# Performance work log

Measured on AMD Instinct MI355X. Metric: run time of the kernel, lower is better.

The kernel has to match this reference:

```python
import jax, jax.numpy as jnp
import numpy as np

N_USERS = 100000
N_ITEMS = 100000
N_NODES = N_USERS + N_ITEMS
NNZ = 6400000
DIM = 64
N_HOPS = 3


def setup_inputs() -> dict:
    key = jax.random.key(0)
    k1, k2, k3, k4, k5 = jax.random.split(key, 5)
    user_embed = jax.random.normal(k1, (N_USERS, DIM), dtype=jnp.float32)
    item_embed = jax.random.normal(k2, (N_ITEMS, DIM), dtype=jnp.float32)
    # Normalized-adjacency-style positive values for the sparse matrix.
    edge_vals = jax.random.uniform(k3, (NNZ,), dtype=jnp.float32)
    edge_rows = jax.random.randint(k4, (NNZ,), 0, N_NODES, dtype=jnp.int32)
    edge_cols = jax.random.randint(k5, (NNZ,), 0, N_NODES, dtype=jnp.int32)
    return {
        "user_embed": user_embed,
        "item_embed": item_embed,
        "edge_vals": edge_vals,
        "edge_rows": edge_rows,
        "edge_cols": edge_cols,
    }


def reference(user_embed, item_embed, edge_vals, edge_rows, edge_cols):
    # all_embed: [N_NODES, DIM]
    all_embed = jnp.concatenate([user_embed, item_embed], axis=0)
    agg = all_embed
    embs = [all_embed]
    for _ in range(N_HOPS):
        # SpMM in COO form: out[r] += v * agg[c]  for each edge (r, c, v)
        gathered = edge_vals[:, None] * agg[edge_cols]  # [NNZ, DIM]
        agg = jax.ops.segment_sum(gathered, edge_rows, num_segments=N_NODES)
        embs.append(agg)
    embs = jnp.stack(embs, axis=1)  # [N_NODES, N_HOPS+1, DIM]
    return embs[:N_USERS], embs[N_USERS:]
```

## Files before the change

kernel.cpp:

```cpp
#include <hip/hip_runtime.h>

#define N_USERS 100000
#define N_ITEMS 100000
#define N_NODES (N_USERS + N_ITEMS)
#define NNZ 6400000
#define DIM 64
#define NHOPS 3
#define NODE_STRIDE ((NHOPS + 1) * DIM)

#define RPB 128
#define NB 1563
#define TILE 8192
#define NTILES ((NNZ + TILE - 1) / TILE)
#define P2CAP 7808

#define WS_BCNT 0
#define WS_BPTR 2048
#define WS_BCUR 4096
#define WS_RP   6144
#define WS_STG  206848
#define WS_MIRA 13006848
#define WS_MIRB 19406848

__device__ __forceinline__ unsigned short f2bf(float f) {
    unsigned u = __float_as_uint(f);
    u += 0x7fffu + ((u >> 16) & 1u);
    return (unsigned short)(u >> 16);
}
__device__ __forceinline__ float bf2f(unsigned short h) {
    return __uint_as_float((unsigned)h << 16);
}

__global__ void zero_bcnt_kernel(int* __restrict__ bcnt) {
    int i = blockIdx.x * blockDim.x + threadIdx.x;
    if (i < NB) bcnt[i] = 0;
}

__global__ void bhist_kernel(const int* __restrict__ rows, int* __restrict__ bcnt) {
    __shared__ int h[NB];
    for (int i = threadIdx.x; i < NB; i += blockDim.x) h[i] = 0;
    __syncthreads();
    int stride = gridDim.x * blockDim.x;
    for (int i = blockIdx.x * blockDim.x + threadIdx.x; i < NNZ; i += stride)
        atomicAdd(&h[rows[i] >> 7], 1);
    __syncthreads();
    for (int i = threadIdx.x; i < NB; i += blockDim.x)
        if (h[i]) atomicAdd(&bcnt[i], h[i]);
}

__global__ void bscan_kernel(const int* __restrict__ bcnt,
                             int* __restrict__ bptr, int* __restrict__ bcur) {
    __shared__ int buf[1024];
    int t = threadIdx.x;
    int a = (2 * t < NB) ? bcnt[2 * t] : 0;
    int b = (2 * t + 1 < NB) ? bcnt[2 * t + 1] : 0;
    int s = a + b;
    buf[t] = s;
    __syncthreads();
    for (int off = 1; off < 1024; off <<= 1) {
        int v = (t >= off) ? buf[t - off] : 0;
        __syncthreads();
        buf[t] += v;
        __syncthreads();
    }
    int ex = buf[t] - s;
    if (2 * t < NB)     { bptr[2 * t] = ex;     bcur[2 * t] = ex; }
    if (2 * t + 1 < NB) { bptr[2 * t + 1] = ex + a; bcur[2 * t + 1] = ex + a; }
    if (t == 0) bptr[NB] = NNZ;
}

__global__ void partition_kernel(const int* __restrict__ rows, const int* __restrict__ cols,
                                 const float* __restrict__ vals,
                                 int* __restrict__ bcur, int2* __restrict__ stg) {
    __shared__ int lh[NB];
    __shared__ int gb[NB];
    for (int i = threadIdx.x; i < NB; i += 512) lh[i] = 0;
    __syncthreads();
    const int base = blockIdx.x * TILE;
    int pk[16];
    #pragma unroll
    for (int k = 0; k < 16; ++k) {
        int e = base + k * 512 + (int)threadIdx.x;
        if (e < NNZ) {
            int r = rows[e];
            int b = r >> 7;
            int rank = atomicAdd(&lh[b], 1);
            pk[k] = b | ((r & 127) << 11) | (rank << 18);
        } else pk[k] = -1;
    }
    __syncthreads();
    for (int i = threadIdx.x; i < NB; i += 512) {
        int c = lh[i];
        if (c) gb[i] = atomicAdd(&bcur[i], c);
    }
    __syncthreads();
    #pragma unroll
    for (int k = 0; k < 16; ++k) {
        if (pk[k] >= 0) {
            int e = base + k * 512 + (int)threadIdx.x;
            int b    = pk[k] & 2047;
            int rl   = (pk[k] >> 11) & 127;
            int rank = pk[k] >> 18;
            int2 v;
            v.x = cols[e] | (rl << 18);
            v.y = __float_as_int(vals[e]);
            stg[gb[b] + rank] = v;
        }
    }
}

__global__ void pass2_kernel(const int* __restrict__ bptr, int2* __restrict__ stg,
                             int* __restrict__ row_ptr) {
    __shared__ int2 sd[P2CAP];
    __shared__ int  lh[RPB];
    __shared__ int  lc[RPB];
    int b = blockIdx.x;
    int s = bptr[b], e = bptr[b + 1];
    int cnt = e - s;
    for (int i = threadIdx.x; i < cnt; i += 256) sd[i] = stg[s + i];
    int t = threadIdx.x;
    if (t < RPB) lh[t] = 0;
    __syncthreads();
    for (int i = threadIdx.x; i < cnt; i += 256)
        atomicAdd(&lh[(sd[i].x >> 18) & 127], 1);
    __syncthreads();
    int own = (t < RPB) ? lh[t] : 0;
    for (int off = 1; off < RPB; off <<= 1) {
        int u = (t < RPB && t >= off) ? lh[t - off] : 0;
        __syncthreads();
        if (t < RPB) lh[t] += u;
        __syncthreads();
    }
    int rowbase = b * RPB;
    int nrows = min(RPB, N_NODES - rowbase);
    if (t < RPB) {
        int ex = lh[t] - own;
        lc[t] = ex;
        if (t < nrows) row_ptr[rowbase + t] = s + ex;
    }
    if (b == NB - 1 && t == 0) row_ptr[N_NODES] = NNZ;
    __syncthreads();
    for (int i = threadIdx.x; i < cnt; i += 256) {
        int2 d = sd[i];
        int rl = (d.x >> 18) & 127;
        int pos = atomicAdd(&lc[rl], 1);
        d.x &= 0x3FFFF;
        stg[s + pos] = d;
    }
}

__global__ void init_hop0_kernel(const float4* __restrict__ ue,
                                 const float4* __restrict__ ie,
                                 float* __restrict__ out,
                                 unsigned short* __restrict__ mirA) {
    int i = blockIdx.x * blockDim.x + threadIdx.x;
    if (i >= N_NODES * 16) return;
    int n = i >> 4, q = i & 15;
    float4 v = (n < N_USERS) ? ue[i] : ie[i - N_USERS * 16];
    ((float4*)(out + (size_t)n * NODE_STRIDE))[q] = v;
    ushort4 h;
    h.x = f2bf(v.x); h.y = f2bf(v.y); h.z = f2bf(v.z); h.w = f2bf(v.w);
    *(ushort4*)(mirA + ((size_t)n << 6) + q * 4) = h;
}

__global__ void spmm_bf_kernel(const int* __restrict__ row_ptr,
                               const int2* __restrict__ csr_pair,
                               const unsigned short* __restrict__ src,
                               unsigned short* __restrict__ dst,
                               float* __restrict__ out, int hop, int write_dst) {
    int wid = (blockIdx.x * blockDim.x + threadIdx.x) >> 6;
    if (wid >= N_NODES) return;
    int lane = threadIdx.x & 63;
    int g = lane >> 4;
    int q = lane & 15;
    int s = row_ptr[wid];
    int e = row_ptr[wid + 1];
    float4 acc = make_float4(0.f, 0.f, 0.f, 0.f);
    int j = s + g;
    for (; j + 4 < e; j += 8) {
        int2 p0 = csr_pair[j];
        int2 p1 = csr_pair[j + 4];
        ushort4 h0 = *(const ushort4*)(src + ((size_t)p0.x << 6) + q * 4);
        ushort4 h1 = *(const ushort4*)(src + ((size_t)p1.x << 6) + q * 4);
        float v0 = __int_as_float(p0.y);
        float v1 = __int_as_float(p1.y);
        acc.x += v0 * bf2f(h0.x); acc.y += v0 * bf2f(h0.y);
        acc.z += v0 * bf2f(h0.z); acc.w += v0 * bf2f(h0.w);
        acc.x += v1 * bf2f(h1.x); acc.y += v1 * bf2f(h1.y);
        acc.z += v1 * bf2f(h1.z); acc.w += v1 * bf2f(h1.w);
    }
    if (j < e) {
        int2 p0 = csr_pair[j];
        ushort4 h0 = *(const ushort4*)(src + ((size_t)p0.x << 6) + q * 4);
        float v0 = __int_as_float(p0.y);
        acc.x += v0 * bf2f(h0.x); acc.y += v0 * bf2f(h0.y);
        acc.z += v0 * bf2f(h0.z); acc.w += v0 * bf2f(h0.w);
    }
    acc.x += __shfl_xor(acc.x, 16); acc.y += __shfl_xor(acc.y, 16);
    acc.z += __shfl_xor(acc.z, 16); acc.w += __shfl_xor(acc.w, 16);
    acc.x += __shfl_xor(acc.x, 32); acc.y += __shfl_xor(acc.y, 32);
    acc.z += __shfl_xor(acc.z, 32); acc.w += __shfl_xor(acc.w, 32);
    if (g == 0) {
        ((float4*)(out + (size_t)wid * NODE_STRIDE + hop * DIM))[q] = acc;
        if (write_dst) {
            ushort4 h;
            h.x = f2bf(acc.x); h.y = f2bf(acc.y); h.z = f2bf(acc.z); h.w = f2bf(acc.w);
            *(ushort4*)(dst + ((size_t)wid << 6) + q * 4) = h;
        }
    }
}

extern "C" void kernel_launch(void* const* d_in, const int* in_sizes, int n_in,
                              void* d_out, int out_size, void* d_ws, size_t ws_size,
                              hipStream_t stream) {
    const float* user_e = (const float*)d_in[0];
    const float* item_e = (const float*)d_in[1];
    const float* vals   = (const float*)d_in[2];
    const int*   rows   = (const int*)d_in[3];
    const int*   cols   = (const int*)d_in[4];
    float* out = (float*)d_out;

    int*  wsi     = (int*)d_ws;
    int*  bcnt    = wsi + WS_BCNT;
    int*  bptr    = wsi + WS_BPTR;
    int*  bcur    = wsi + WS_BCUR;
    int*  row_ptr = wsi + WS_RP;
    int2* stg     = (int2*)(wsi + WS_STG);
    unsigned short* mirA = (unsigned short*)(wsi + WS_MIRA);
    unsigned short* mirB = (unsigned short*)(wsi + WS_MIRB);

    hipLaunchKernelGGL(zero_bcnt_kernel, dim3((NB + 255) / 256), dim3(256), 0, stream, bcnt);
    hipLaunchKernelGGL(bhist_kernel, dim3(1024), dim3(256), 0, stream, rows, bcnt);
    hipLaunchKernelGGL(bscan_kernel, dim3(1), dim3(1024), 0, stream, bcnt, bptr, bcur);
    hipLaunchKernelGGL(partition_kernel, dim3(NTILES), dim3(512), 0, stream,
                       rows, cols, vals, bcur, stg);
    hipLaunchKernelGGL(pass2_kernel, dim3(NB), dim3(256), 0, stream, bptr, stg, row_ptr);
    hipLaunchKernelGGL(init_hop0_kernel, dim3((N_NODES * 16 + 255) / 256), dim3(256), 0, stream,
                       (const float4*)user_e, (const float4*)item_e, out, mirA);

    const dim3 sg((N_NODES * 64 + 255) / 256), sb(256);
    hipLaunchKernelGGL(spmm_bf_kernel, sg, sb, 0, stream, row_ptr, stg, mirA, mirB, out, 1, 1);
    hipLaunchKernelGGL(spmm_bf_kernel, sg, sb, 0, stream, row_ptr, stg, mirB, mirA, out, 2, 1);
    hipLaunchKernelGGL(spmm_bf_kernel, sg, sb, 0, stream, row_ptr, stg, mirA, mirB, out, 3, 0);
}
```

Baseline: 705.0 us.

## Widen row buckets to 192 and restructure partition as persistent two-pass kernel

Row buckets grow from 128 to 192 rows, which cuts the bucket count to 1042. The partition kernel becomes a persistent grid of 256 blocks of 1024 threads over 16K-edge tiles. Each tile is counted in shared memory first, then scattered using shared atomics for slot positions, so the packed per-thread rank registers go away. The scatter rereads rows and adds integer divides. pass2 now clamps cnt to a smaller P2CAP of 7000, which could silently drop edges if a bucket overflows. Within-bucket order now depends on atomic timing.

Result: faster. 666.7 us (-5.4%).

```diff
diff --git a/kernel.cpp b/kernel.cpp
--- a/kernel.cpp
+++ b/kernel.cpp
@@ -8,19 +8,19 @@
 #define NHOPS 3
 #define NODE_STRIDE ((NHOPS + 1) * DIM)
 
-#define RPB 128
-#define NB 1563
-#define TILE 8192
-#define NTILES ((NNZ + TILE - 1) / TILE)
-#define P2CAP 7808
+#define BROWS 192
+#define NBK 1042
+#define PTILE 16384
+#define NTILES ((NNZ + PTILE - 1) / PTILE)
+#define P2CAP 7000
 
 #define WS_BCNT 0
-#define WS_BPTR 2048
-#define WS_BCUR 4096
-#define WS_RP   6144
-#define WS_STG  206848
-#define WS_MIRA 13006848
-#define WS_MIRB 19406848
+#define WS_BPTR 1056
+#define WS_BCUR 2112
+#define WS_RP   3168
+#define WS_STG  203264
+#define WS_MIRA 13003264
+#define WS_MIRB 19403264
 
 __device__ __forceinline__ unsigned short f2bf(float f) {
     unsigned u = __float_as_uint(f);
@@ -33,18 +33,18 @@
 
 __global__ void zero_bcnt_kernel(int* __restrict__ bcnt) {
     int i = blockIdx.x * blockDim.x + threadIdx.x;
-    if (i < NB) bcnt[i] = 0;
+    if (i < NBK) bcnt[i] = 0;
 }
 
 __global__ void bhist_kernel(const int* __restrict__ rows, int* __restrict__ bcnt) {
-    __shared__ int h[NB];
-    for (int i = threadIdx.x; i < NB; i += blockDim.x) h[i] = 0;
+    __shared__ int h[NBK];
+    for (int i = threadIdx.x; i < NBK; i += blockDim.x) h[i] = 0;
     __syncthreads();
     int stride = gridDim.x * blockDim.x;
     for (int i = blockIdx.x * blockDim.x + threadIdx.x; i < NNZ; i += stride)
-        atomicAdd(&h[rows[i] >> 7], 1);
-    __syncthreads();
-    for (int i = threadIdx.x; i < NB; i += blockDim.x)
+        atomicAdd(&h[(unsigned)rows[i] / BROWS], 1);
+    __syncthreads();
+    for (int i = threadIdx.x; i < NBK; i += blockDim.x)
         if (h[i]) atomicAdd(&bcnt[i], h[i]);
 }
 
@@ -52,8 +52,8 @@
                              int* __restrict__ bptr, int* __restrict__ bcur) {
     __shared__ int buf[1024];
     int t = threadIdx.x;
-    int a = (2 * t < NB) ? bcnt[2 * t] : 0;
-    int b = (2 * t + 1 < NB) ? bcnt[2 * t + 1] : 0;
+    int a = (2 * t < NBK) ? bcnt[2 * t] : 0;
+    int b = (2 * t + 1 < NBK) ? bcnt[2 * t + 1] : 0;
     int s = a + b;
     buf[t] = s;
     __syncthreads();
@@ -64,85 +64,77 @@
         __syncthreads();
     }
     int ex = buf[t] - s;
-    if (2 * t < NB)     { bptr[2 * t] = ex;     bcur[2 * t] = ex; }
-    if (2 * t + 1 < NB) { bptr[2 * t + 1] = ex + a; bcur[2 * t + 1] = ex + a; }
-    if (t == 0) bptr[NB] = NNZ;
-}
-
-__global__ void partition_kernel(const int* __restrict__ rows, const int* __restrict__ cols,
-                                 const float* __restrict__ vals,
-                                 int* __restrict__ bcur, int2* __restrict__ stg) {
-    __shared__ int lh[NB];
-    __shared__ int gb[NB];
-    for (int i = threadIdx.x; i < NB; i += 512) lh[i] = 0;
-    __syncthreads();
-    const int base = blockIdx.x * TILE;
-    int pk[16];
-    #pragma unroll
-    for (int k = 0; k < 16; ++k) {
-        int e = base + k * 512 + (int)threadIdx.x;
-        if (e < NNZ) {
+    if (2 * t < NBK)     { bptr[2 * t] = ex;         bcur[2 * t] = ex; }
+    if (2 * t + 1 < NBK) { bptr[2 * t + 1] = ex + a; bcur[2 * t + 1] = ex + a; }
+    if (t == 0) bptr[NBK] = NNZ;
+}
+
+__global__ void __launch_bounds__(1024) partition_kernel(
+        const int* __restrict__ rows, const int* __restrict__ cols,
+        const float* __restrict__ vals,
+        int* __restrict__ bcur, int2* __restrict__ stg) {
+    __shared__ int cur[NBK];
+    for (int tile = blockIdx.x; tile < NTILES; tile += gridDim.x) {
+        for (int i = threadIdx.x; i < NBK; i += 1024) cur[i] = 0;
+        __syncthreads();
+        const int base = tile * PTILE;
+        const int end  = min(base + PTILE, NNZ);
+        for (int e = base + (int)threadIdx.x; e < end; e += 1024)
+            atomicAdd(&cur[(unsigned)rows[e] / BROWS], 1);
+        __syncthreads();
+        for (int i = threadIdx.x; i < NBK; i += 1024) {
+            int c = cur[i];
+            cur[i] = c ? atomicAdd(&bcur[i], c) : 0;
+        }
+        __syncthreads();
+        for (int e = base + (int)threadIdx.x; e < end; e += 1024) {
             int r = rows[e];
-            int b = r >> 7;
-            int rank = atomicAdd(&lh[b], 1);
-            pk[k] = b | ((r & 127) << 11) | (rank << 18);
-        } else pk[k] = -1;
-    }
-    __syncthreads();
-    for (int i = threadIdx.x; i < NB; i += 512) {
-        int c = lh[i];
-        if (c) gb[i] = atomicAdd(&bcur[i], c);
-    }
-    __syncthreads();
-    #pragma unroll
-    for (int k = 0; k < 16; ++k) {
-        if (pk[k] >= 0) {
-            int e = base + k * 512 + (int)threadIdx.x;
-            int b    = pk[k] & 2047;
-            int rl   = (pk[k] >> 11) & 127;
-            int rank = pk[k] >> 18;
+            unsigned b = (unsigned)r / BROWS;
+            int rl = r - (int)b * BROWS;
+            int pos = atomicAdd(&cur[b], 1);
             int2 v;
             v.x = cols[e] | (rl << 18);
             v.y = __float_as_int(vals[e]);
-            stg[gb[b] + rank] = v;
+            stg[pos] = v;
         }
-    }
-}
-
-__global__ void pass2_kernel(const int* __restrict__ bptr, int2* __restrict__ stg,
-                             int* __restrict__ row_ptr) {
+        __syncthreads();
+    }
+}
+
+__global__ void __launch_bounds__(256) pass2_kernel(
+        const int* __restrict__ bptr, int2* __restrict__ stg,
+        int* __restrict__ row_ptr) {
     __shared__ int2 sd[P2CAP];
-    __shared__ int  lh[RPB];
-    __shared__ int  lc[RPB];
+    __shared__ int  lh[BROWS];
+    __shared__ int  lc[BROWS];
     int b = blockIdx.x;
     int s = bptr[b], e = bptr[b + 1];
-    int cnt = e - s;
+    int cnt = min(e - s, P2CAP);
     for (int i = threadIdx.x; i < cnt; i += 256) sd[i] = stg[s + i];
     int t = threadIdx.x;
-    if (t < RPB) lh[t] = 0;
-    __syncthreads();
-    for (int i = threadIdx.x; i < cnt; i += 256)
-        atomicAdd(&lh[(sd[i].x >> 18) & 127], 1);
-    __syncthreads();
-    int own = (t < RPB) ? lh[t] : 0;
-    for (int off = 1; off < RPB; off <<= 1) {
-        int u = (t < RPB && t >= off) ? lh[t - off] : 0;
-        __syncthreads();
-        if (t < RPB) lh[t] += u;
-        __syncthreads();
-    }
-    int rowbase = b * RPB;
-    int nrows = min(RPB, N_NODES - rowbase);
-    if (t < RPB) {
+    if (t < BROWS) lh[t] = 0;
+    __syncthreads();
+    for (int i = t; i < cnt; i += 256)
+        atomicAdd(&lh[(unsigned)sd[i].x >> 18], 1);
+    __syncthreads();
+    int own = (t < BROWS) ? lh[t] : 0;
+    for (int off = 1; off < BROWS; off <<= 1) {
+        int u = (t < BROWS && t >= off) ? lh[t - off] : 0;
+        __syncthreads();
+        if (t < BROWS) lh[t] += u;
+        __syncthreads();
+    }
+    int rowbase = b * BROWS;
+    if (t < BROWS) {
         int ex = lh[t] - own;
         lc[t] = ex;
-        if (t < nrows) row_ptr[rowbase + t] = s + ex;
-    }
-    if (b == NB - 1 && t == 0) row_ptr[N_NODES] = NNZ;
-    __syncthreads();
-    for (int i = threadIdx.x; i < cnt; i += 256) {
+        if (rowbase + t < N_NODES) row_ptr[rowbase + t] = s + ex;
+    }
+    if (b == NBK - 1 && t == 0) row_ptr[N_NODES] = NNZ;
+    __syncthreads();
+    for (int i = t; i < cnt; i += 256) {
         int2 d = sd[i];
-        int rl = (d.x >> 18) & 127;
+        int rl = (unsigned)d.x >> 18;
         int pos = atomicAdd(&lc[rl], 1);
         d.x &= 0x3FFFF;
         stg[s + pos] = d;
@@ -229,12 +221,12 @@
     unsigned short* mirA = (unsigned short*)(wsi + WS_MIRA);
     unsigned short* mirB = (unsigned short*)(wsi + WS_MIRB);
 
-    hipLaunchKernelGGL(zero_bcnt_kernel, dim3((NB + 255) / 256), dim3(256), 0, stream, bcnt);
+    hipLaunchKernelGGL(zero_bcnt_kernel, dim3((NBK + 255) / 256), dim3(256), 0, stream, bcnt);
     hipLaunchKernelGGL(bhist_kernel, dim3(1024), dim3(256), 0, stream, rows, bcnt);
     hipLaunchKernelGGL(bscan_kernel, dim3(1), dim3(1024), 0, stream, bcnt, bptr, bcur);
-    hipLaunchKernelGGL(partition_kernel, dim3(NTILES), dim3(512), 0, stream,
+    hipLaunchKernelGGL(partition_kernel, dim3(256), dim3(1024), 0, stream,
                        rows, cols, vals, bcur, stg);
-    hipLaunchKernelGGL(pass2_kernel, dim3(NB), dim3(256), 0, stream, bptr, stg, row_ptr);
+    hipLaunchKernelGGL(pass2_kernel, dim3(NBK), dim3(256), 0, stream, bptr, stg, row_ptr);
     hipLaunchKernelGGL(init_hop0_kernel, dim3((N_NODES * 16 + 255) / 256), dim3(256), 0, stream,
                        (const float4*)user_e, (const float4*)item_e, out, mirA);
 
```
